# Optimization experiments

Hardware: AMD Instinct MI355X
Metric: run time of the kernel (lower is better)

The kernel has to match this reference:

```python
import jax, jax.numpy as jnp
import numpy as np

IN_C, OUT_C, HEADS = 128, 256, 8
HEAD_DIM = OUT_C // HEADS


def setup_inputs() -> dict:
    key = jax.random.key(0)
    ks = jax.random.split(key, 20)
    B, N, K = 4, 4096, 16
    s = lambda k, shape, fan_in: jax.random.normal(k, shape, jnp.float32) / np.sqrt(fan_in)
    return {
        "center_xyz": jax.random.normal(ks[0], (B, N, 3), jnp.float32),
        "center_features": jax.random.normal(ks[1], (B, N, IN_C), jnp.float32),
        "neigh_xyz": jax.random.normal(ks[2], (B, N, K, 3), jnp.float32),
        "neigh_feat": jax.random.normal(ks[3], (B, N, K, IN_C), jnp.float32),
        # weights stored as (in, out) so y = x @ W + b matches torch Linear math
        "Wq": s(ks[4], (IN_C, OUT_C), IN_C), "bq": jnp.zeros((OUT_C,), jnp.float32),
        "Wk": s(ks[5], (IN_C, OUT_C), IN_C), "bk": jnp.zeros((OUT_C,), jnp.float32),
        "Wv": s(ks[6], (IN_C, OUT_C), IN_C), "bv": jnp.zeros((OUT_C,), jnp.float32),
        "Wp1": s(ks[7], (4, OUT_C), 4), "bp1": jnp.zeros((OUT_C,), jnp.float32),
        "Wp2": s(ks[8], (OUT_C, OUT_C), OUT_C), "bp2": jnp.zeros((OUT_C,), jnp.float32),
        "Wo": s(ks[9], (OUT_C, OUT_C), OUT_C), "bo": jnp.zeros((OUT_C,), jnp.float32),
        "Wr": s(ks[10], (IN_C, OUT_C), IN_C), "br": jnp.zeros((OUT_C,), jnp.float32),
    }


def reference(center_xyz, center_features, neigh_xyz, neigh_feat,
              Wq, bq, Wk, bk, Wv, bv, Wp1, bp1, Wp2, bp2, Wo, bo, Wr, br):
    B, N, _ = center_features.shape
    K = neigh_feat.shape[2]
    H, D = HEADS, HEAD_DIM

    rel_pos = neigh_xyz - center_xyz[:, :, None, :]                 # (B,N,K,3)
    rel_dist = jnp.linalg.norm(rel_pos, axis=-1, keepdims=True)     # (B,N,K,1)
    pos_in = jnp.concatenate([rel_pos, rel_dist], axis=-1)          # (B,N,K,4)
    pos_enc = jax.nn.relu(pos_in @ Wp1 + bp1) @ Wp2 + bp2           # (B,N,K,OUT_C)

    q = (center_features @ Wq + bq).reshape(B, N, H, D)             # (B,N,H,D)
    k = (neigh_feat @ Wk + bk).reshape(B, N, K, H, D)
    v = (neigh_feat @ Wv + bv).reshape(B, N, K, H, D)
    pe = pos_enc.reshape(B, N, K, H, D)
    k = k + pe
    v = v + pe

    scores = jnp.einsum('bnhd,bnkhd->bnhk', q, k) / np.sqrt(D)      # (B,N,H,K)
    attn = jax.nn.softmax(scores, axis=-1)
    attn_out = jnp.einsum('bnhk,bnkhd->bnhd', attn, v).reshape(B, N, H * D)

    out = attn_out @ Wo + bo + (center_features @ Wr + br)
    return jnp.where(out >= 0, out, 0.2 * out)  # leaky_relu(0.2)
```

## Files before the change

kernel.cpp:

```cpp
#include <hip/hip_runtime.h>
#include <hip/hip_bf16.h>

typedef __attribute__((ext_vector_type(8))) __bf16 bf16x8;
typedef __attribute__((ext_vector_type(4))) float f32x4;

#define OFF_BLOB 0
#define OFF_WQ   131072
#define OFF_WO   163840
#define OFF_WR   229376

__device__ __forceinline__ f32x4 mfma16(bf16x8 a, bf16x8 b, f32x4 c) {
    return __builtin_amdgcn_mfma_f32_16x16x32_bf16(a, b, c, 0, 0, 0);
}
__device__ __forceinline__ bf16x8 ldb16(const short* p) { return *(const bf16x8*)p; }

union BfBits { __bf16 b; short s; };
__device__ __forceinline__ short f2b(float x) { BfBits u; u.b = (__bf16)x; return u.s; }
__device__ __forceinline__ float b2f(short x) { BfBits u; u.s = x; return (float)u.b; }

__device__ __forceinline__ void gload_lds16(const short* g, short* l) {
    __builtin_amdgcn_global_load_lds(
        (const __attribute__((address_space(1))) unsigned int*)g,
        (__attribute__((address_space(3))) unsigned int*)l, 16, 0, 0);
}

__global__ void prep_kernel(const float* __restrict__ Wq, const float* __restrict__ Wk,
                            const float* __restrict__ Wv, const float* __restrict__ Wp2,
                            const float* __restrict__ Wo, const float* __restrict__ Wr,
                            short* __restrict__ o) {
    int t = blockIdx.x * 256 + threadIdx.x;
    float v;
    if (t < 131072) {
        int h = t >> 14, r = t & 16383, set = r >> 9, li = r & 511;
        int lane = li >> 3, e = li & 7;
        int l15 = lane & 15, grp = lane >> 4;
        const float* src; int kc;
        if (set < 16)      { src = Wp2; kc = set >> 1; }
        else if (set < 24) { src = Wk;  kc = (set - 16) >> 1; }
        else               { src = Wv;  kc = (set - 24) >> 1; }
        int nt = set & 1;
        int n = h * 32 + nt * 16 + l15;
        int k = kc * 32 + grp * 8 + e;
        v = src[k * 256 + n];
    } else if (t < 163840) {
        int i = t - 131072, n = i >> 7, k = i & 127;
        v = Wq[k * 256 + n];
    } else if (t < 229376) {
        int i = t - 163840, n = i >> 8, k = i & 255;
        v = Wo[k * 256 + n];
    } else {
        int i = t - 229376, n = i >> 7, k = i & 127;
        v = Wr[k * 256 + n];
    }
    o[t] = f2b(v);
}

__global__ __launch_bounds__(512, 2) void fused_kernel(
    const float* __restrict__ cxyz, const float* __restrict__ cfeat,
    const float* __restrict__ nxyz, const float* __restrict__ nfeat,
    const float* __restrict__ bq,  const float* __restrict__ bk,
    const float* __restrict__ bv,  const float* __restrict__ Wp1,
    const float* __restrict__ bp1, const float* __restrict__ bp2,
    const float* __restrict__ bo,  const float* __restrict__ br,
    const short* __restrict__ wsb, float* __restrict__ out)
{
    __shared__ short sWBuf[2][16384];
    __shared__ short sQh[16][256];
    __shared__ short sAOh[16][256];
    __shared__ float sBkv[256], sBvv[256];
    __shared__ float sNx[768];
    __shared__ float sCx[48];
    float* sWp1b = (float*)&sWBuf[1][0];

    const int t = threadIdx.x;
    const int bid = blockIdx.x;
    const int w = t >> 6, lane = t & 63, grp = lane >> 4, l15 = lane & 15;

    {
        const short* src = wsb + OFF_BLOB;
        #pragma unroll
        for (int i = 0; i < 4; ++i) {
            int s = w * 4 + i;
            gload_lds16(src + s * 512 + lane * 8, &sWBuf[0][s * 512]);
        }
    }

    {
        if (t < 256) {
            float p2 = bp2[t];
            sBkv[t] = bk[t] + p2;
            sBvv[t] = bv[t] + p2;
            sWp1b[t*8+0] = Wp1[t];
            sWp1b[t*8+1] = Wp1[256 + t];
            sWp1b[t*8+2] = Wp1[512 + t];
            sWp1b[t*8+3] = Wp1[768 + t];
            sWp1b[t*8+4] = bp1[t];
        }
        sNx[t] = nxyz[bid * 768 + t];
        if (t < 256) sNx[512 + t] = nxyz[bid * 768 + 512 + t];
        if (t < 48)  sCx[t] = cxyz[bid * 48 + t];
    }
    __syncthreads();

    float pin[2][4];
    #pragma unroll
    for (int mt = 0; mt < 2; ++mt) {
        int row = w*32 + mt*16 + l15;
        int cl = row >> 4;
        float rx = sNx[row*3+0] - sCx[cl*3+0];
        float ry = sNx[row*3+1] - sCx[cl*3+1];
        float rz = sNx[row*3+2] - sCx[cl*3+2];
        pin[mt][0] = rx; pin[mt][1] = ry; pin[mt][2] = rz;
        pin[mt][3] = sqrtf(rx*rx + ry*ry + rz*rz);
    }

    bf16x8 h1f[2][8];
    #pragma unroll
    for (int kc = 0; kc < 8; ++kc) {
        bf16x8 f0, f1;
        #pragma unroll
        for (int e = 0; e < 8; ++e) {
            const float* wp = &sWp1b[(kc*32 + grp*8 + e) * 8];
            float w0 = wp[0], w1 = wp[1], w2 = wp[2], w3 = wp[3], bb = wp[4];
            float a = fmaf(pin[0][0],w0, fmaf(pin[0][1],w1, fmaf(pin[0][2],w2, fmaf(pin[0][3],w3, bb))));
            float b = fmaf(pin[1][0],w0, fmaf(pin[1][1],w1, fmaf(pin[1][2],w2, fmaf(pin[1][3],w3, bb))));
            f0[e] = (__bf16)fmaxf(a, 0.f);
            f1[e] = (__bf16)fmaxf(b, 0.f);
        }
        h1f[0][kc] = f0; h1f[1][kc] = f1;
    }

    bf16x8 xnf[2][4];
    #pragma unroll
    for (int mt = 0; mt < 2; ++mt) {
        int grow = bid*256 + w*32 + mt*16 + l15;
        const float* pbase = nfeat + grow*128 + grp*8;
        #pragma unroll
        for (int kc = 0; kc < 4; ++kc) {
            const float* p = pbase + kc*32;
            f32x4 a = *(const f32x4*)p;
            f32x4 c = *(const f32x4*)(p + 4);
            bf16x8 v;
            v[0]=(__bf16)a[0]; v[1]=(__bf16)a[1]; v[2]=(__bf16)a[2]; v[3]=(__bf16)a[3];
            v[4]=(__bf16)c[0]; v[5]=(__bf16)c[1]; v[6]=(__bf16)c[2]; v[7]=(__bf16)c[3];
            xnf[mt][kc] = v;
        }
    }

    {
        bf16x8 xcf[4];
        int gc = bid*16 + l15;
        const float* pbase = cfeat + gc*128 + grp*8;
        #pragma unroll
        for (int kc = 0; kc < 4; ++kc) {
            const float* p = pbase + kc*32;
            f32x4 a = *(const f32x4*)p;
            f32x4 c = *(const f32x4*)(p + 4);
            bf16x8 v;
            v[0]=(__bf16)a[0]; v[1]=(__bf16)a[1]; v[2]=(__bf16)a[2]; v[3]=(__bf16)a[3];
            v[4]=(__bf16)c[0]; v[5]=(__bf16)c[1]; v[6]=(__bf16)c[2]; v[7]=(__bf16)c[3];
            xcf[kc] = v;
        }
        const short* wqT = wsb + OFF_WQ;
        #pragma unroll
        for (int ntl = 0; ntl < 2; ++ntl) {
            int n = (w*2 + ntl)*16 + l15;
            f32x4 acc = {0.f, 0.f, 0.f, 0.f};
            #pragma unroll
            for (int kc = 0; kc < 4; ++kc)
                acc = mfma16(xcf[kc], ldb16(wqT + n*128 + kc*32 + grp*8), acc);
            float bqn = bq[n];
            #pragma unroll
            for (int r = 0; r < 4; ++r) {
                int m = grp*4 + r;
                sQh[m][n] = f2b((acc[r] + bqn) * 0.1767766952966369f);
            }
        }
    }
    __syncthreads();

    #pragma unroll 1
    for (int h = 0; h < 8; ++h) {
        const short* cw = sWBuf[h & 1];
        if (h < 7) {
            short* dst = sWBuf[(h + 1) & 1];
            const short* src = wsb + OFF_BLOB + (h + 1) * 16384;
            #pragma unroll
            for (int i = 0; i < 4; ++i) {
                int s = w * 4 + i;
                gload_lds16(src + s * 512 + lane * 8, dst + s * 512);
            }
        }
        const int hb = h * 32;

        f32x4 pe[2][2];
        {
            f32x4 z = {0.f, 0.f, 0.f, 0.f};
            pe[0][0]=z; pe[0][1]=z; pe[1][0]=z; pe[1][1]=z;
        }
        #pragma unroll
        for (int kc = 0; kc < 8; ++kc) {
            #pragma unroll
            for (int nt = 0; nt < 2; ++nt) {
                bf16x8 bw = ldb16(cw + (kc*2 + nt)*512 + lane*8);
                pe[0][nt] = mfma16(h1f[0][kc], bw, pe[0][nt]);
                pe[1][nt] = mfma16(h1f[1][kc], bw, pe[1][nt]);
            }
        }

        f32x4 ka[2][2], va[2][2];
        ka[0][0]=pe[0][0]; ka[0][1]=pe[0][1]; ka[1][0]=pe[1][0]; ka[1][1]=pe[1][1];
        va[0][0]=pe[0][0]; va[0][1]=pe[0][1]; va[1][0]=pe[1][0]; va[1][1]=pe[1][1];
        #pragma unroll
        for (int kc = 0; kc < 4; ++kc) {
            #pragma unroll
            for (int nt = 0; nt < 2; ++nt) {
                bf16x8 wk8 = ldb16(cw + (16 + kc*2 + nt)*512 + lane*8);
                bf16x8 wv8 = ldb16(cw + (24 + kc*2 + nt)*512 + lane*8);
                #pragma unroll
                for (int mt = 0; mt < 2; ++mt) {
                    ka[mt][nt] = mfma16(xnf[mt][kc], wk8, ka[mt][nt]);
                    va[mt][nt] = mfma16(xnf[mt][kc], wv8, va[mt][nt]);
                }
            }
        }

        float bkv0 = sBkv[hb + l15], bkv1 = sBkv[hb + 16 + l15];
        float bvv0 = sBvv[hb + l15], bvv1 = sBvv[hb + 16 + l15];

        #pragma unroll
        for (int mt = 0; mt < 2; ++mt) {
            float q0 = b2f(sQh[2*w + mt][hb + l15]);
            float q1 = b2f(sQh[2*w + mt][hb + 16 + l15]);
            float sp[4];
            #pragma unroll
            for (int r = 0; r < 4; ++r)
                sp[r] = q0*(ka[mt][0][r] + bkv0) + q1*(ka[mt][1][r] + bkv1);
            #pragma unroll
            for (int msk = 1; msk < 16; msk <<= 1) {
                sp[0] += __shfl_xor(sp[0], msk);
                sp[1] += __shfl_xor(sp[1], msk);
                sp[2] += __shfl_xor(sp[2], msk);
                sp[3] += __shfl_xor(sp[3], msk);
            }
            float mx = fmaxf(fmaxf(sp[0], sp[1]), fmaxf(sp[2], sp[3]));
            mx = fmaxf(mx, __shfl_xor(mx, 16));
            mx = fmaxf(mx, __shfl_xor(mx, 32));
            const float l2e = 1.4426950408889634f;
            float p0 = exp2f((sp[0]-mx)*l2e);
            float p1 = exp2f((sp[1]-mx)*l2e);
            float p2 = exp2f((sp[2]-mx)*l2e);
            float p3 = exp2f((sp[3]-mx)*l2e);
            float sm = (p0+p1) + (p2+p3);
            sm += __shfl_xor(sm, 16);
            sm += __shfl_xor(sm, 32);
            float inv = 1.0f / sm;
            p0 *= inv; p1 *= inv; p2 *= inv; p3 *= inv;
            #pragma unroll
            for (int nt = 0; nt < 2; ++nt) {
                float ov = p0*va[mt][nt][0] + p1*va[mt][nt][1]
                         + p2*va[mt][nt][2] + p3*va[mt][nt][3];
                ov += __shfl_xor(ov, 16);
                ov += __shfl_xor(ov, 32);
                if (grp == 0) sAOh[2*w + mt][hb + nt*16 + l15] = f2b(ov + (nt ? bvv1 : bvv0));
            }
        }
        __syncthreads();
    }

    const short* woT = wsb + OFF_WO;
    const short* wrT = wsb + OFF_WR;
    bf16x8 aof[8];
    #pragma unroll
    for (int kc = 0; kc < 8; ++kc)
        aof[kc] = ldb16(&sAOh[l15][kc*32 + grp*8]);
    bf16x8 xcf[4];
    {
        int gc = bid*16 + l15;
        const float* pbase = cfeat + gc*128 + grp*8;
        #pragma unroll
        for (int kc = 0; kc < 4; ++kc) {
            const float* p = pbase + kc*32;
            f32x4 a = *(const f32x4*)p;
            f32x4 c = *(const f32x4*)(p + 4);
            bf16x8 v;
            v[0]=(__bf16)a[0]; v[1]=(__bf16)a[1]; v[2]=(__bf16)a[2]; v[3]=(__bf16)a[3];
            v[4]=(__bf16)c[0]; v[5]=(__bf16)c[1]; v[6]=(__bf16)c[2]; v[7]=(__bf16)c[3];
            xcf[kc] = v;
        }
    }
    #pragma unroll
    for (int ntl = 0; ntl < 2; ++ntl) {
        int n = (w*2 + ntl)*16 + l15;
        f32x4 acc = {0.f, 0.f, 0.f, 0.f};
        #pragma unroll
        for (int kc = 0; kc < 8; ++kc)
            acc = mfma16(aof[kc], ldb16(woT + n*256 + kc*32 + grp*8), acc);
        #pragma unroll
        for (int kc = 0; kc < 4; ++kc)
            acc = mfma16(xcf[kc], ldb16(wrT + n*128 + kc*32 + grp*8), acc);
        float bb = bo[n] + br[n];
        #pragma unroll
        for (int r = 0; r < 4; ++r) {
            int m = grp*4 + r;
            float v = acc[r] + bb;
            out[(bid*16 + m)*256 + n] = (v >= 0.f) ? v : 0.2f*v;
        }
    }
}

extern "C" void kernel_launch(void* const* d_in, const int* in_sizes, int n_in,
                              void* d_out, int out_size, void* d_ws, size_t ws_size,
                              hipStream_t stream) {
    const float* cxyz  = (const float*)d_in[0];
    const float* cfeat = (const float*)d_in[1];
    const float* nxyz  = (const float*)d_in[2];
    const float* nfeat = (const float*)d_in[3];
    const float* Wq  = (const float*)d_in[4];
    const float* bq  = (const float*)d_in[5];
    const float* Wk  = (const float*)d_in[6];
    const float* bk  = (const float*)d_in[7];
    const float* Wv  = (const float*)d_in[8];
    const float* bv  = (const float*)d_in[9];
    const float* Wp1 = (const float*)d_in[10];
    const float* bp1 = (const float*)d_in[11];
    const float* Wp2 = (const float*)d_in[12];
    const float* bp2 = (const float*)d_in[13];
    const float* Wo  = (const float*)d_in[14];
    const float* bo  = (const float*)d_in[15];
    const float* Wr  = (const float*)d_in[16];
    const float* br  = (const float*)d_in[17];
    short* wsb = (short*)d_ws;

    if (ws_size < 262144 * sizeof(short)) return;

    prep_kernel<<<1024, 256, 0, stream>>>(Wq, Wk, Wv, Wp2, Wo, Wr, wsb);
    fused_kernel<<<1024, 512, 0, stream>>>(cxyz, cfeat, nxyz, nfeat,
        bq, bk, bv, Wp1, bp1, bp2, bo, br, wsb, (float*)d_out);
}
```

Baseline: 178.9 us.

## Replace double-buffered per-head weight loads with a 3-slot half-head LDS ring

Splits each head's weight blob into two halves (PE weights and K/V weights) and streams them through a 3-slot LDS ring using global_load_lds. Explicit vmcnt waits plus s_barrier replace the per-head __syncthreads, so the next half's load can overlap the current half's MFMA work. It also reduces the weight LDS footprint from 64KB to 48KB. The tradeoff is an extra barrier per head, and correctness now depends on hand-counted vmcnt values, with the Wp1 scratch aliasing ring slot 2.

```diff
diff --git a/kernel.cpp b/kernel.cpp
--- a/kernel.cpp
+++ b/kernel.cpp
@@ -22,6 +22,17 @@
     __builtin_amdgcn_global_load_lds(
         (const __attribute__((address_space(1))) unsigned int*)g,
         (__attribute__((address_space(3))) unsigned int*)l, 16, 0, 0);
+}
+
+__device__ __forceinline__ void vmw_bar2() {
+    __builtin_amdgcn_sched_barrier(0);
+    asm volatile("s_waitcnt vmcnt(2)" ::: "memory");
+    __builtin_amdgcn_s_barrier();
+}
+__device__ __forceinline__ void vmw_bar0() {
+    __builtin_amdgcn_sched_barrier(0);
+    asm volatile("s_waitcnt vmcnt(0)" ::: "memory");
+    __builtin_amdgcn_s_barrier();
 }
 
 __global__ void prep_kernel(const float* __restrict__ Wq, const float* __restrict__ Wk,
@@ -64,26 +75,30 @@
     const float* __restrict__ bo,  const float* __restrict__ br,
     const short* __restrict__ wsb, float* __restrict__ out)
 {
-    __shared__ short sWBuf[2][16384];
+    __shared__ short sRing[3][8192];
     __shared__ short sQh[16][256];
     __shared__ short sAOh[16][256];
     __shared__ float sBkv[256], sBvv[256];
     __shared__ float sNx[768];
     __shared__ float sCx[48];
-    float* sWp1b = (float*)&sWBuf[1][0];
+    float* sWp1b = (float*)&sRing[2][0];
 
     const int t = threadIdx.x;
     const int bid = blockIdx.x;
     const int w = t >> 6, lane = t & 63, grp = lane >> 4, l15 = lane & 15;
 
-    {
-        const short* src = wsb + OFF_BLOB;
-        #pragma unroll
-        for (int i = 0; i < 4; ++i) {
-            int s = w * 4 + i;
-            gload_lds16(src + s * 512 + lane * 8, &sWBuf[0][s * 512]);
-        }
-    }
+    auto issue_half = [&](int q, int slot) {
+        const short* src = wsb + OFF_BLOB + (q >> 1) * 16384 + (q & 1) * 8192;
+        short* dst = &sRing[slot][0];
+        #pragma unroll
+        for (int i = 0; i < 2; ++i) {
+            int s = w * 2 + i;
+            gload_lds16(src + s * 512 + lane * 8, dst + s * 512);
+        }
+    };
+
+    issue_half(0, 0);
+    issue_half(1, 1);
 
     {
         if (t < 256) {
@@ -179,20 +194,15 @@
     }
     __syncthreads();
 
+    int slPE = 0, slKV = 1, slNx = 2;
     #pragma unroll 1
     for (int h = 0; h < 8; ++h) {
-        const short* cw = sWBuf[h & 1];
-        if (h < 7) {
-            short* dst = sWBuf[(h + 1) & 1];
-            const short* src = wsb + OFF_BLOB + (h + 1) * 16384;
-            #pragma unroll
-            for (int i = 0; i < 4; ++i) {
-                int s = w * 4 + i;
-                gload_lds16(src + s * 512 + lane * 8, dst + s * 512);
-            }
-        }
         const int hb = h * 32;
-
+        const short* cpe = &sRing[slPE][0];
+        const short* ckv = &sRing[slKV][0];
+
+        vmw_bar2();
+        if (h < 7) issue_half(2*h + 2, slNx);
         f32x4 pe[2][2];
         {
             f32x4 z = {0.f, 0.f, 0.f, 0.f};
@@ -202,12 +212,14 @@
         for (int kc = 0; kc < 8; ++kc) {
             #pragma unroll
             for (int nt = 0; nt < 2; ++nt) {
-                bf16x8 bw = ldb16(cw + (kc*2 + nt)*512 + lane*8);
+                bf16x8 bw = ldb16(cpe + (kc*2 + nt)*512 + lane*8);
                 pe[0][nt] = mfma16(h1f[0][kc], bw, pe[0][nt]);
                 pe[1][nt] = mfma16(h1f[1][kc], bw, pe[1][nt]);
             }
         }
 
+        if (h < 7) { vmw_bar2(); issue_half(2*h + 3, slPE); }
+        else       { vmw_bar0(); }
         f32x4 ka[2][2], va[2][2];
         ka[0][0]=pe[0][0]; ka[0][1]=pe[0][1]; ka[1][0]=pe[1][0]; ka[1][1]=pe[1][1];
         va[0][0]=pe[0][0]; va[0][1]=pe[0][1]; va[1][0]=pe[1][0]; va[1][1]=pe[1][1];
@@ -215,8 +227,8 @@
         for (int kc = 0; kc < 4; ++kc) {
             #pragma unroll
             for (int nt = 0; nt < 2; ++nt) {
-                bf16x8 wk8 = ldb16(cw + (16 + kc*2 + nt)*512 + lane*8);
-                bf16x8 wv8 = ldb16(cw + (24 + kc*2 + nt)*512 + lane*8);
+                bf16x8 wk8 = ldb16(ckv + (kc*2 + nt)*512 + lane*8);
+                bf16x8 wv8 = ldb16(ckv + (8 + kc*2 + nt)*512 + lane*8);
                 #pragma unroll
                 for (int mt = 0; mt < 2; ++mt) {
                     ka[mt][nt] = mfma16(xnf[mt][kc], wk8, ka[mt][nt]);
@@ -265,8 +277,10 @@
                 if (grp == 0) sAOh[2*w + mt][hb + nt*16 + l15] = f2b(ov + (nt ? bvv1 : bvv0));
             }
         }
-        __syncthreads();
-    }
+
+        int t0 = slNx; slNx = slKV; slKV = slPE; slPE = t0;
+    }
+    __syncthreads();
 
     const short* woT = wsb + OFF_WO;
     const short* wrT = wsb + OFF_WR;
```

After: 204.7 us. 1.14x slower.
